# Optimization experiments

Measured on AMD Instinct MI355X. Metric: run time of the kernel, lower is better.

## Reference

```python
import jax, jax.numpy as jnp
import numpy as np

N_NODES = 50000
N_EDGES = 800000
F_IN, F_HID, F_OUT = 128, 64, 32


def setup_inputs() -> dict:
    key = jax.random.key(0)
    k1, k2, k3, k4, k5, k6 = jax.random.split(key, 6)
    x = jax.random.normal(k1, (N_NODES, F_IN), dtype=jnp.float32)
    edge_index = jax.random.randint(k2, (2, N_EDGES), 0, N_NODES, dtype=jnp.int64)
    # Glorot-ish init for the two GCNConv linear layers
    W1 = jax.random.normal(k3, (F_IN, F_HID), dtype=jnp.float32) / np.sqrt(F_IN)
    b1 = jnp.zeros((F_HID,), dtype=jnp.float32)
    W2 = jax.random.normal(k4, (F_HID, F_OUT), dtype=jnp.float32) / np.sqrt(F_HID)
    b2 = jnp.zeros((F_OUT,), dtype=jnp.float32)
    return {"x": x, "edge_index": edge_index, "W1": W1, "b1": b1, "W2": W2, "b2": b2}


def _gcn_conv(x, src, dst, norm, W, b):
    # GCNConv: linear transform, then D^{-1/2}(A+I)D^{-1/2} aggregation
    xw = x @ W                                # [N, F_out]
    msg = xw[src] * norm[:, None]             # [E+N, F_out] gather + scale
    out = jax.ops.segment_sum(msg, dst, num_segments=x.shape[0])
    return out + b


def reference(x, edge_index, W1, b1, W2, b2):
    n = x.shape[0]
    self_loops = jnp.arange(n, dtype=edge_index.dtype)
    src = jnp.concatenate([edge_index[0], self_loops])  # [E+N]
    dst = jnp.concatenate([edge_index[1], self_loops])
    # symmetric degree normalization (self-loops guarantee deg >= 1)
    deg = jax.ops.segment_sum(jnp.ones_like(dst, dtype=x.dtype), dst, num_segments=n)
    dinv = jax.lax.rsqrt(deg)
    norm = dinv[src] * dinv[dst]              # [E+N]

    h = _gcn_conv(x, src, dst, norm, W1, b1)
    h = jax.nn.relu(h)
    # dropout p=0.5 is identity in eval mode (training=False)
    out = _gcn_conv(h, src, dst, norm, W2, b2)
    return out
```

## Files before the change

kernel.cpp:

```cpp
#include <hip/hip_runtime.h>
#include <hip/hip_fp16.h>

#define NN 50000
#define NE 800000
#define F_IN 128
#define F_HID 64
#define F_OUT 32
#define CAP 48
#define NBUCK 196
#define EPB 4096
#define CELL 64
#define NXW1 782

typedef _Float16 f16x8 __attribute__((ext_vector_type(8)));
typedef float f32x4 __attribute__((ext_vector_type(4)));
#define XS_STR 136


__global__ __launch_bounds__(256) void fused_xw1_partition_kernel(
        const float* __restrict__ x, const float* __restrict__ W,
        const int* __restrict__ src, const int* __restrict__ dst,
        int* __restrict__ cnt2t, unsigned int* __restrict__ bstore2,
        __half* __restrict__ outh) {
    __shared__ _Float16 xs[64 * XS_STR];
    __shared__ _Float16 wt[64 * XS_STR];
    __shared__ int hist[4][NBUCK];
    __shared__ int cur[NBUCK];
    int t = threadIdx.x;

    if (blockIdx.x < NBUCK) {
        int blk = blockIdx.x;
        for (int i = t; i < 4 * NBUCK; i += 256) ((int*)hist)[i] = 0;
        __syncthreads();
        int wv = t >> 6;
        int base = blk * EPB;
        unsigned int pk[16];
#pragma unroll
        for (int i = 0; i < 16; ++i) {
            int e = base + i * 256 + t;
            if (e < NE) {
                unsigned int d = (unsigned int)dst[e];
                unsigned int s = (unsigned int)src[e];
                pk[i] = (d << 16) | s;
                atomicAdd(&hist[wv][d >> 8], 1);
            } else {
                pk[i] = 0xFFFFFFFFu;
            }
        }
        __syncthreads();
        for (int b = t; b < NBUCK; b += 256) {
            int h = hist[0][b] + hist[1][b] + hist[2][b] + hist[3][b];
            cur[b] = 0;
            cnt2t[b * NBUCK + blk] = h;
        }
        __syncthreads();
#pragma unroll
        for (int i = 0; i < 16; ++i) {
            unsigned int p = pk[i];
            if (p != 0xFFFFFFFFu) {
                int b = p >> 24;
                int pos = atomicAdd(&cur[b], 1);
                if (pos < CELL) bstore2[((size_t)blk * NBUCK + b) * CELL + pos] = p;
            }
        }
        return;
    }

    int node0 = (blockIdx.x - NBUCK) * 64;

    {
        int r = t >> 2;
        int c0 = (t & 3) * 32;
        int gn = node0 + r;
        if (gn > NN - 1) gn = NN - 1;
        const float4* xrow = (const float4*)(x + (size_t)gn * F_IN);
#pragma unroll
        for (int i = 0; i < 8; ++i) {
            float4 v = xrow[(c0 >> 2) + i];
            _Float16* p = &xs[r * XS_STR + c0 + i * 4];
            p[0] = (_Float16)v.x; p[1] = (_Float16)v.y;
            p[2] = (_Float16)v.z; p[3] = (_Float16)v.w;
        }
    }
#pragma unroll
    for (int i = 0; i < 8; ++i) {
        int idx4 = t + i * 256;
        int k = idx4 >> 4;
        int n0 = (idx4 & 15) << 2;
        float4 v = ((const float4*)W)[idx4];
        wt[(n0 + 0) * XS_STR + k] = (_Float16)v.x;
        wt[(n0 + 1) * XS_STR + k] = (_Float16)v.y;
        wt[(n0 + 2) * XS_STR + k] = (_Float16)v.z;
        wt[(n0 + 3) * XS_STR + k] = (_Float16)v.w;
    }
    __syncthreads();

    int wave = t >> 6;
    int l = t & 63;
    int quad = l >> 4;
    int lm = l & 15;

    f32x4 acc[4] = {{0,0,0,0},{0,0,0,0},{0,0,0,0},{0,0,0,0}};
    const _Float16* abase = &xs[(wave * 16 + lm) * XS_STR + quad * 8];
#pragma unroll
    for (int kk4 = 0; kk4 < 4; ++kk4) {
        int kk = kk4 * 32;
        f16x8 a = *(const f16x8*)(abase + kk);
#pragma unroll
        for (int ft = 0; ft < 4; ++ft) {
            f16x8 b = *(const f16x8*)&wt[(ft * 16 + lm) * XS_STR + kk + quad * 8];
            acc[ft] = __builtin_amdgcn_mfma_f32_16x16x32_f16(a, b, acc[ft], 0, 0, 0);
        }
    }

    __syncthreads();
    _Float16* ot = xs;
#pragma unroll
    for (int ft = 0; ft < 4; ++ft) {
#pragma unroll
        for (int r = 0; r < 4; ++r) {
            int row_l = wave * 16 + quad * 4 + r;
            ot[row_l * 64 + ft * 16 + lm] = (_Float16)acc[ft][r];
        }
    }
    __syncthreads();
#pragma unroll
    for (int i = 0; i < 2; ++i) {
        int idx = t + i * 256;
        int row = idx >> 3;
        int c8 = (idx & 7) * 8;
        int gn = node0 + row;
        if (gn < NN)
            *(uint4*)(outh + (size_t)gn * 64 + c8) = *(const uint4*)&ot[row * 64 + c8];
    }
}


__device__ __forceinline__ void slot_insert(unsigned int p, int* cnt_l,
                                            unsigned short* slot_l) {
    int dl = (p >> 16) & 255;
    int pos = atomicAdd(&cnt_l[dl], 1);
    if (pos < CAP) slot_l[dl * CAP + pos] = (unsigned short)(p & 0xFFFFu);
}

__global__ __launch_bounds__(256) void build_slots_kernel(
        const int* __restrict__ cnt2t, const unsigned int* __restrict__ bstore2,
        unsigned short* __restrict__ slot, int* __restrict__ cnt_g, float* __restrict__ dinv) {
    __shared__ unsigned short slot_l[256 * CAP];
    __shared__ int cnt_l[256];
    int t = threadIdx.x;
    int b = blockIdx.x;
    cnt_l[t] = 0;
    __syncthreads();

    for (int blk = t; blk < NBUCK; blk += 256) {
        int c = cnt2t[b * NBUCK + blk];
        if (c > CELL) c = CELL;
        const unsigned int* seg = bstore2 + ((size_t)blk * NBUCK + b) * CELL;
        int j = 0;
        for (; j + 4 <= c; j += 4) {
            unsigned int p0 = seg[j + 0];
            unsigned int p1 = seg[j + 1];
            unsigned int p2 = seg[j + 2];
            unsigned int p3 = seg[j + 3];
            slot_insert(p0, cnt_l, slot_l);
            slot_insert(p1, cnt_l, slot_l);
            slot_insert(p2, cnt_l, slot_l);
            slot_insert(p3, cnt_l, slot_l);
        }
        for (; j < c; ++j) slot_insert(seg[j], cnt_l, slot_l);
    }
    __syncthreads();

    unsigned int* sg = (unsigned int*)(slot + (size_t)b * 256 * CAP);
    const unsigned int* sl = (const unsigned int*)slot_l;
    for (int j = t; j < 256 * CAP / 2; j += 256) sg[j] = sl[j];

    int n = b * 256 + t;
    if (n < NN) {
        int c = cnt_l[t];
        cnt_g[n] = c;
        dinv[n] = rsqrtf(1.0f + (float)c);
    }
}


__global__ __launch_bounds__(256) void gather64_w2_kernel(
        const __half* __restrict__ xw, const int* __restrict__ cnt,
        const unsigned short* __restrict__ slot, const float* __restrict__ dinv,
        const float* __restrict__ b1, const float* __restrict__ W2,
        __half* __restrict__ hw2h) {
    __shared__ float w2s[F_HID * F_OUT];
    __shared__ float hl[4][F_HID];
    __shared__ float psum[128];
    int t = threadIdx.x;
    for (int i = t; i < F_HID * F_OUT / 4; i += 256)
        ((float4*)w2s)[i] = ((const float4*)W2)[i];

    int lane = t & 63;
    int wv = t >> 6;
    int n = blockIdx.x * 4 + wv;
    int st = lane >> 4;
    int fl4 = lane & 15;
    const uint2* base = (const uint2*)xw;
    int deg = cnt[n];
    if (deg > CAP) deg = CAP;
    const unsigned short* srow = slot + (size_t)n * CAP;
    float a0 = 0, a1 = 0, a2 = 0, a3 = 0;
    int e = st;
    for (; e + 4 < deg; e += 8) {
        int s0 = srow[e];
        int s1 = srow[e + 4];
        float dv0 = dinv[s0], dv1 = dinv[s1];
        uint2 u0 = base[(size_t)s0 * 16 + fl4];
        uint2 u1 = base[(size_t)s1 * 16 + fl4];
        float2 p0 = __half22float2(*(__half2*)&u0.x);
        float2 p1 = __half22float2(*(__half2*)&u0.y);
        float2 q0 = __half22float2(*(__half2*)&u1.x);
        float2 q1 = __half22float2(*(__half2*)&u1.y);
        a0 += dv0 * p0.x + dv1 * q0.x;
        a1 += dv0 * p0.y + dv1 * q0.y;
        a2 += dv0 * p1.x + dv1 * q1.x;
        a3 += dv0 * p1.y + dv1 * q1.y;
    }
    for (; e < deg; e += 4) {
        int s = srow[e];
        float dv = dinv[s];
        uint2 u = base[(size_t)s * 16 + fl4];
        float2 p0 = __half22float2(*(__half2*)&u.x);
        float2 p1 = __half22float2(*(__half2*)&u.y);
        a0 += dv * p0.x; a1 += dv * p0.y; a2 += dv * p1.x; a3 += dv * p1.y;
    }
    a0 += __shfl_xor(a0, 16, 64); a1 += __shfl_xor(a1, 16, 64);
    a2 += __shfl_xor(a2, 16, 64); a3 += __shfl_xor(a3, 16, 64);
    a0 += __shfl_xor(a0, 32, 64); a1 += __shfl_xor(a1, 32, 64);
    a2 += __shfl_xor(a2, 32, 64); a3 += __shfl_xor(a3, 32, 64);
    if (st == 0) {
        float di = dinv[n];
        uint2 u = base[(size_t)n * 16 + fl4];
        float2 s0 = __half22float2(*(__half2*)&u.x);
        float2 s1 = __half22float2(*(__half2*)&u.y);
        float4 bb = ((const float4*)b1)[fl4];
        float v0 = di * (a0 + di * s0.x) + bb.x;
        float v1 = di * (a1 + di * s0.y) + bb.y;
        float v2 = di * (a2 + di * s1.x) + bb.z;
        float v3 = di * (a3 + di * s1.y) + bb.w;
        float* hr = &hl[wv][fl4 * 4];
        hr[0] = v0 > 0.f ? v0 : 0.f;
        hr[1] = v1 > 0.f ? v1 : 0.f;
        hr[2] = v2 > 0.f ? v2 : 0.f;
        hr[3] = v3 > 0.f ? v3 : 0.f;
    }
    __syncthreads();
    {
        int half = t >> 7;
        int idx = t & 127;
        int nq = idx >> 5;
        int f = idx & 31;
        const float* hr = hl[nq];
        int k0 = half * 32;
        float acc = 0.0f;
#pragma unroll
        for (int k = 0; k < 32; ++k) acc += hr[k0 + k] * w2s[(k0 + k) * F_OUT + f];
        if (half) psum[idx] = acc;
        __syncthreads();
        if (!half) {
            int gn = blockIdx.x * 4 + nq;
            hw2h[(size_t)gn * F_OUT + f] = __float2half((acc + psum[idx]) * dinv[gn]);
        }
    }
}


__global__ __launch_bounds__(256) void gather32_kernel(
        const __half* __restrict__ scaled, const int* __restrict__ cnt,
        const unsigned short* __restrict__ slot, const float* __restrict__ dinv,
        const float* __restrict__ bias, float* __restrict__ out) {
    int lane = threadIdx.x & 63;
    int n = blockIdx.x * 4 + (threadIdx.x >> 6);
    if (n >= NN) return;
    int st = lane >> 3;
    int fl4 = lane & 7;
    const uint2* base = (const uint2*)scaled;
    int deg = cnt[n];
    if (deg > CAP) deg = CAP;
    const unsigned short* srow = slot + (size_t)n * CAP;
    float a0 = 0, a1 = 0, a2 = 0, a3 = 0;
    int e = st;
    for (; e + 8 < deg; e += 16) {
        int s0 = srow[e];
        int s1 = srow[e + 8];
        uint2 u0 = base[(size_t)s0 * 8 + fl4];
        uint2 u1 = base[(size_t)s1 * 8 + fl4];
        float2 p0 = __half22float2(*(__half2*)&u0.x);
        float2 p1 = __half22float2(*(__half2*)&u0.y);
        float2 q0 = __half22float2(*(__half2*)&u1.x);
        float2 q1 = __half22float2(*(__half2*)&u1.y);
        a0 += p0.x + q0.x; a1 += p0.y + q0.y;
        a2 += p1.x + q1.x; a3 += p1.y + q1.y;
    }
    for (; e < deg; e += 8) {
        int s = srow[e];
        uint2 u = base[(size_t)s * 8 + fl4];
        float2 p0 = __half22float2(*(__half2*)&u.x);
        float2 p1 = __half22float2(*(__half2*)&u.y);
        a0 += p0.x; a1 += p0.y; a2 += p1.x; a3 += p1.y;
    }
    a0 += __shfl_xor(a0, 8, 64);  a1 += __shfl_xor(a1, 8, 64);
    a2 += __shfl_xor(a2, 8, 64);  a3 += __shfl_xor(a3, 8, 64);
    a0 += __shfl_xor(a0, 16, 64); a1 += __shfl_xor(a1, 16, 64);
    a2 += __shfl_xor(a2, 16, 64); a3 += __shfl_xor(a3, 16, 64);
    a0 += __shfl_xor(a0, 32, 64); a1 += __shfl_xor(a1, 32, 64);
    a2 += __shfl_xor(a2, 32, 64); a3 += __shfl_xor(a3, 32, 64);
    if (st == 0) {
        uint2 u = base[(size_t)n * 8 + fl4];
        float2 s0 = __half22float2(*(__half2*)&u.x);
        float2 s1 = __half22float2(*(__half2*)&u.y);
        float4 b4 = ((const float4*)bias)[fl4];
        float di = dinv[n];
        float4 r;
        r.x = di * (a0 + s0.x) + b4.x;
        r.y = di * (a1 + s0.y) + b4.y;
        r.z = di * (a2 + s1.x) + b4.z;
        r.w = di * (a3 + s1.y) + b4.w;
        ((float4*)out)[(size_t)n * 8 + fl4] = r;
    }
}


extern "C" void kernel_launch(void* const* d_in, const int* in_sizes, int n_in,
                              void* d_out, int out_size, void* d_ws, size_t ws_size,
                              hipStream_t stream) {
    const float* x  = (const float*)d_in[0];
    const int*   ei = (const int*)d_in[1];
    const float* W1 = (const float*)d_in[2];
    const float* b1 = (const float*)d_in[3];
    const float* W2 = (const float*)d_in[4];
    const float* b2 = (const float*)d_in[5];
    const int* src = ei;
    const int* dst = ei + NE;

    float*          ws      = (float*)d_ws;
    float*          dinv    = ws;
    int*            cnt     = (int*)(ws + 50048);
    int*            cnt2t   = (int*)(ws + 100096);
    unsigned int*   bstore2 = (unsigned int*)(ws + 138624);
    unsigned short* slot    = (unsigned short*)(ws + 2597248);
    __half*         xw1h    = (__half*)(ws + 3801472);
    __half*         hw2h    = (__half*)(ws + 5401472);
    float*          out     = (float*)d_out;

    fused_xw1_partition_kernel<<<NBUCK + NXW1, 256, 0, stream>>>(
        x, W1, src, dst, cnt2t, bstore2, xw1h);
    build_slots_kernel<<<NBUCK, 256, 0, stream>>>(cnt2t, bstore2, slot, cnt, dinv);
    gather64_w2_kernel<<<NN / 4, 256, 0, stream>>>(xw1h, cnt, slot, dinv, b1, W2, hw2h);
    gather32_kernel<<<NN / 4, 256, 0, stream>>>(hw2h, cnt, slot, dinv, b2, out);
}
```

Before: 151.8 us.

## Unroll layer-1 gather to four edges and make W2 matvec wave-local

The layer-1 gather now unrolls to four independent neighbor loads per iteration so more memory requests are in flight per lane. The block-wide barrier and shared partial-sum buffer used for the W2 product are replaced by a per-wave computation, with a cross-half shuffle reduction and a wait on local memory counters. dinv[n] is loaded once early, and launch-bound occupancy hints are added to both gather kernels. Correctness now depends on the inline wait making the per-wave shared-memory writes visible without a barrier, and the wider unroll raises register pressure.

```diff
diff --git a/kernel.cpp b/kernel.cpp
--- a/kernel.cpp
+++ b/kernel.cpp
@@ -185,17 +185,17 @@
 }
 
 
-__global__ __launch_bounds__(256) void gather64_w2_kernel(
+__global__ __launch_bounds__(256, 4) void gather64_w2_kernel(
         const __half* __restrict__ xw, const int* __restrict__ cnt,
         const unsigned short* __restrict__ slot, const float* __restrict__ dinv,
         const float* __restrict__ b1, const float* __restrict__ W2,
         __half* __restrict__ hw2h) {
     __shared__ float w2s[F_HID * F_OUT];
     __shared__ float hl[4][F_HID];
-    __shared__ float psum[128];
     int t = threadIdx.x;
     for (int i = t; i < F_HID * F_OUT / 4; i += 256)
         ((float4*)w2s)[i] = ((const float4*)W2)[i];
+    __syncthreads();
 
     int lane = t & 63;
     int wv = t >> 6;
@@ -205,23 +205,28 @@
     const uint2* base = (const uint2*)xw;
     int deg = cnt[n];
     if (deg > CAP) deg = CAP;
+    float din = dinv[n];
     const unsigned short* srow = slot + (size_t)n * CAP;
     float a0 = 0, a1 = 0, a2 = 0, a3 = 0;
     int e = st;
-    for (; e + 4 < deg; e += 8) {
+    for (; e + 12 < deg; e += 16) {
         int s0 = srow[e];
         int s1 = srow[e + 4];
-        float dv0 = dinv[s0], dv1 = dinv[s1];
+        int s2 = srow[e + 8];
+        int s3 = srow[e + 12];
+        float dv0 = dinv[s0], dv1 = dinv[s1], dv2 = dinv[s2], dv3 = dinv[s3];
         uint2 u0 = base[(size_t)s0 * 16 + fl4];
         uint2 u1 = base[(size_t)s1 * 16 + fl4];
-        float2 p0 = __half22float2(*(__half2*)&u0.x);
-        float2 p1 = __half22float2(*(__half2*)&u0.y);
-        float2 q0 = __half22float2(*(__half2*)&u1.x);
-        float2 q1 = __half22float2(*(__half2*)&u1.y);
-        a0 += dv0 * p0.x + dv1 * q0.x;
-        a1 += dv0 * p0.y + dv1 * q0.y;
-        a2 += dv0 * p1.x + dv1 * q1.x;
-        a3 += dv0 * p1.y + dv1 * q1.y;
+        uint2 u2 = base[(size_t)s2 * 16 + fl4];
+        uint2 u3 = base[(size_t)s3 * 16 + fl4];
+        float2 p0 = __half22float2(*(__half2*)&u0.x), p1 = __half22float2(*(__half2*)&u0.y);
+        float2 q0 = __half22float2(*(__half2*)&u1.x), q1 = __half22float2(*(__half2*)&u1.y);
+        float2 r0 = __half22float2(*(__half2*)&u2.x), r1 = __half22float2(*(__half2*)&u2.y);
+        float2 t0 = __half22float2(*(__half2*)&u3.x), t1 = __half22float2(*(__half2*)&u3.y);
+        a0 += dv0 * p0.x + dv1 * q0.x + dv2 * r0.x + dv3 * t0.x;
+        a1 += dv0 * p0.y + dv1 * q0.y + dv2 * r0.y + dv3 * t0.y;
+        a2 += dv0 * p1.x + dv1 * q1.x + dv2 * r1.x + dv3 * t1.x;
+        a3 += dv0 * p1.y + dv1 * q1.y + dv2 * r1.y + dv3 * t1.y;
     }
     for (; e < deg; e += 4) {
         int s = srow[e];
@@ -236,43 +241,35 @@
     a0 += __shfl_xor(a0, 32, 64); a1 += __shfl_xor(a1, 32, 64);
     a2 += __shfl_xor(a2, 32, 64); a3 += __shfl_xor(a3, 32, 64);
     if (st == 0) {
-        float di = dinv[n];
         uint2 u = base[(size_t)n * 16 + fl4];
         float2 s0 = __half22float2(*(__half2*)&u.x);
         float2 s1 = __half22float2(*(__half2*)&u.y);
         float4 bb = ((const float4*)b1)[fl4];
-        float v0 = di * (a0 + di * s0.x) + bb.x;
-        float v1 = di * (a1 + di * s0.y) + bb.y;
-        float v2 = di * (a2 + di * s1.x) + bb.z;
-        float v3 = di * (a3 + di * s1.y) + bb.w;
+        float v0 = din * (a0 + din * s0.x) + bb.x;
+        float v1 = din * (a1 + din * s0.y) + bb.y;
+        float v2 = din * (a2 + din * s1.x) + bb.z;
+        float v3 = din * (a3 + din * s1.y) + bb.w;
         float* hr = &hl[wv][fl4 * 4];
         hr[0] = v0 > 0.f ? v0 : 0.f;
         hr[1] = v1 > 0.f ? v1 : 0.f;
         hr[2] = v2 > 0.f ? v2 : 0.f;
         hr[3] = v3 > 0.f ? v3 : 0.f;
     }
-    __syncthreads();
+    asm volatile("s_waitcnt lgkmcnt(0)" ::: "memory");
     {
-        int half = t >> 7;
-        int idx = t & 127;
-        int nq = idx >> 5;
-        int f = idx & 31;
-        const float* hr = hl[nq];
-        int k0 = half * 32;
+        int f = lane & 31;
+        int kh = lane >> 5;
+        const float* hr = &hl[wv][kh * 32];
         float acc = 0.0f;
 #pragma unroll
-        for (int k = 0; k < 32; ++k) acc += hr[k0 + k] * w2s[(k0 + k) * F_OUT + f];
-        if (half) psum[idx] = acc;
-        __syncthreads();
-        if (!half) {
-            int gn = blockIdx.x * 4 + nq;
-            hw2h[(size_t)gn * F_OUT + f] = __float2half((acc + psum[idx]) * dinv[gn]);
-        }
-    }
-}
-
-
-__global__ __launch_bounds__(256) void gather32_kernel(
+        for (int k = 0; k < 32; ++k) acc += hr[k] * w2s[(kh * 32 + k) * F_OUT + f];
+        acc += __shfl_xor(acc, 32, 64);
+        if (kh == 0) hw2h[(size_t)n * F_OUT + f] = __float2half(acc * din);
+    }
+}
+
+
+__global__ __launch_bounds__(256, 8) void gather32_kernel(
         const __half* __restrict__ scaled, const int* __restrict__ cnt,
         const unsigned short* __restrict__ slot, const float* __restrict__ dinv,
         const float* __restrict__ bias, float* __restrict__ out) {
```

Result: no change. 150.6 us, median of 2 (-0.8%).
